# Kernel tuning notes

Hardware: AMD Instinct MI355X
Metric: run time of the kernel (lower is better)

The kernel has to match this reference:

```python
import jax, jax.numpy as jnp
import numpy as np

DIM = 768
HEADS = 12
HEAD_DIM = DIM // HEADS
EPS = 1e-5


def _layernorm(x, w, b):
    # normalize over last axis (head_dim), affine params shape [head_dim]
    mu = jnp.mean(x, axis=-1, keepdims=True)
    var = jnp.mean(jnp.square(x - mu), axis=-1, keepdims=True)
    return (x - mu) * jax.lax.rsqrt(var + EPS) * w + b


def setup_inputs() -> dict:
    key = jax.random.key(0)
    ks = jax.random.split(key, 8)
    B, N, C = 8, 1024, DIM
    s = 1.0 / np.sqrt(C)
    return {
        "x": jax.random.normal(ks[0], (B, N, C), jnp.float32),
        "qkv_w": jax.random.normal(ks[1], (3 * C, C), jnp.float32) * s,
        "qkv_b": jnp.zeros((3 * C,), jnp.float32),
        "qn_w": jnp.ones((HEAD_DIM,), jnp.float32),
        "qn_b": jnp.zeros((HEAD_DIM,), jnp.float32),
        "kn_w": jnp.ones((HEAD_DIM,), jnp.float32),
        "kn_b": jnp.zeros((HEAD_DIM,), jnp.float32),
        "proj_w": jax.random.normal(ks[2], (C, C), jnp.float32) * s,
        "proj_b": jnp.zeros((C,), jnp.float32),
    }


def reference(x, qkv_w, qkv_b, qn_w, qn_b, kn_w, kn_b, proj_w, proj_b):
    B, N, C = x.shape
    H, D = HEADS, HEAD_DIM
    scale = D ** -0.5
    # qkv projection: [B,N,3C] -> [3,B,H,N,D]
    qkv = (x @ qkv_w.T + qkv_b).reshape(B, N, 3, H, D).transpose(2, 0, 3, 1, 4)
    q, k, v = qkv[0], qkv[1], qkv[2]
    q = _layernorm(q, qn_w, qn_b)
    k = _layernorm(k, kn_w, kn_b)
    # attention scores [B,H,N,N]
    attn = jnp.einsum("bhqd,bhkd->bhqk", q, k) * scale
    attn = jax.nn.softmax(attn, axis=-1)
    out = jnp.einsum("bhqk,bhkd->bhqd", attn, v)  # [B,H,N,D]
    out = out.transpose(0, 2, 1, 3).reshape(B, N, C)
    return out @ proj_w.T + proj_b
```

## Files before the change

### kernel.cpp

```cpp
#include <hip/hip_runtime.h>

#define DIM 768
#define HEADS 12
#define HDIM 64
#define B_ 8
#define N_ 1024
#define EPS 1e-5f
#define QPRE 0.18033688f

typedef __bf16 bf16x8 __attribute__((ext_vector_type(8)));
typedef float  f32x4  __attribute__((ext_vector_type(4)));

using u16 = unsigned short;
using u32 = unsigned int;

static __device__ __forceinline__ u16 f2b_rne(float f){
    u32 u = __float_as_uint(f);
    u += 0x7fffu + ((u >> 16) & 1u);
    return (u16)(u >> 16);
}

static __device__ __forceinline__ void gl_lds16(const void* g, void* l){
    __builtin_amdgcn_global_load_lds(
        (const __attribute__((address_space(1))) unsigned int*)g,
        (__attribute__((address_space(3))) unsigned int*)l, 16, 0, 0);
}

__global__ __launch_bounds__(256) void cast_bf16_kernel(
    const float* __restrict__ in, u16* __restrict__ out, int n8)
{
    int i = blockIdx.x * 256 + threadIdx.x;
    if (i >= n8) return;
    const float4* p = (const float4*)in;
    float4 a = p[2*i], b = p[2*i+1];
    uint4 r;
    r.x = (u32)f2b_rne(a.x) | ((u32)f2b_rne(a.y) << 16);
    r.y = (u32)f2b_rne(a.z) | ((u32)f2b_rne(a.w) << 16);
    r.z = (u32)f2b_rne(b.x) | ((u32)f2b_rne(b.y) << 16);
    r.w = (u32)f2b_rne(b.z) | ((u32)f2b_rne(b.w) << 16);
    ((uint4*)out)[i] = r;
}

__global__ __launch_bounds__(256) void qkv_gemm_ln(
    const u16* __restrict__ xb, const u16* __restrict__ wb,
    const float* __restrict__ bias,
    const float* __restrict__ qn_w, const float* __restrict__ qn_b,
    const float* __restrict__ kn_w, const float* __restrict__ kn_b,
    u16* __restrict__ Q, u16* __restrict__ K, u16* __restrict__ VT)
{
    __shared__ __align__(16) unsigned char Asl[128*128];
    __shared__ __align__(16) unsigned char Bsl[128*128];
    const int t = threadIdx.x;
    const int lane = t & 63, wid = t >> 6;
    const int wr = wid >> 1, wc = wid & 1;
    const int l15 = lane & 15, l4 = lane >> 4;
    const int lr  = lane >> 3;
    const int lcs = ((lane & 7) ^ lr & 7) * 16;
    const int rsw = (l15 & 7) << 4;

    const int b0 = blockIdx.x;
    const int lg = (b0 & 7) * 144 + (b0 >> 3);
    const int col0 = (lg % 18) * 128, row0 = (lg / 18) * 128;

    f32x4 acc[4][4];
    #pragma unroll
    for (int m = 0; m < 4; ++m)
        #pragma unroll
        for (int n = 0; n < 4; ++n) acc[m][n] = f32x4{0.f,0.f,0.f,0.f};

    for (int k0 = 0; k0 < DIM; k0 += 64) {
        __syncthreads();
        #pragma unroll
        for (int c = 0; c < 4; ++c) {
            int rg = wid*32 + c*8;
            gl_lds16((const unsigned char*)xb + (size_t)(row0 + rg + lr)*1536 + k0*2 + lcs,
                     Asl + rg*128);
            gl_lds16((const unsigned char*)wb + (size_t)(col0 + rg + lr)*1536 + k0*2 + lcs,
                     Bsl + rg*128);
        }
        __syncthreads();
        #pragma unroll
        for (int s = 0; s < 2; ++s) {
            bf16x8 af[4], bfr[4];
            #pragma unroll
            for (int m = 0; m < 4; ++m)
                af[m] = *(const bf16x8*)(Asl + (wr*64 + m*16 + l15)*128 + ((l4*16 + s*64) ^ rsw));
            #pragma unroll
            for (int n = 0; n < 4; ++n)
                bfr[n] = *(const bf16x8*)(Bsl + (wc*64 + n*16 + l15)*128 + ((l4*16 + s*64) ^ rsw));
            #pragma unroll
            for (int m = 0; m < 4; ++m)
                #pragma unroll
                for (int n = 0; n < 4; ++n)
                    acc[m][n] = __builtin_amdgcn_mfma_f32_16x16x32_bf16(af[m], bfr[n], acc[m][n], 0, 0, 0);
        }
    }

    const int cg0 = col0 + wc*64;
    const int which = cg0 / DIM;
    const int h = (cg0 % DIM) / HDIM;

    float bias_v[4];
    #pragma unroll
    for (int n = 0; n < 4; ++n) bias_v[n] = bias[cg0 + n*16 + l15];
    #pragma unroll
    for (int m = 0; m < 4; ++m)
        #pragma unroll
        for (int n = 0; n < 4; ++n)
            #pragma unroll
            for (int r = 0; r < 4; ++r) acc[m][n][r] += bias_v[n];

    __syncthreads();
    unsigned char* Tw = (wid < 2 ? Asl : Bsl) + (wid & 1) * 8192;

    if (which < 2) {
        const float* lwp = (which == 0) ? qn_w : kn_w;
        const float* lbp = (which == 0) ? qn_b : kn_b;
        const float qsc = (which == 0) ? QPRE : 1.0f;
        float lw_v[4], lb_v[4];
        #pragma unroll
        for (int n = 0; n < 4; ++n) { lw_v[n] = lwp[n*16 + l15] * qsc; lb_v[n] = lbp[n*16 + l15] * qsc; }

        #pragma unroll
        for (int m = 0; m < 4; ++m)
            #pragma unroll
            for (int r = 0; r < 4; ++r) {
                float s = 0.f, s2 = 0.f;
                #pragma unroll
                for (int n = 0; n < 4; ++n) { float v = acc[m][n][r]; s += v; s2 += v*v; }
                #pragma unroll
                for (int off = 1; off < 16; off <<= 1) {
                    s  += __shfl_xor(s,  off, 64);
                    s2 += __shfl_xor(s2, off, 64);
                }
                float mu  = s * (1.f/64.f);
                float var = s2 * (1.f/64.f) - mu*mu;
                float rs  = rsqrtf(var + EPS);
                #pragma unroll
                for (int n = 0; n < 4; ++n)
                    acc[m][n][r] = (acc[m][n][r] - mu) * rs * lw_v[n] + lb_v[n];
            }

        #pragma unroll
        for (int m = 0; m < 4; ++m)
            #pragma unroll
            for (int n = 0; n < 4; ++n)
                #pragma unroll
                for (int r = 0; r < 4; ++r)
                    *(u16*)(Tw + (m*16 + l4*4 + r)*128 + (n*16 + l15)*2) = f2b_rne(acc[m][n][r]);

        u16* dst = (which == 0) ? Q : K;
        const int tok0 = row0 + wr*64;
        const int b = tok0 >> 10, n0 = tok0 & 1023;
        const size_t bh = (size_t)(b * HEADS + h);
        #pragma unroll
        for (int i = 0; i < 8; ++i) {
            int row = i*8 + (lane >> 3);
            int d0  = (lane & 7) * 8;
            uint4 val = *(const uint4*)(Tw + row*128 + d0*2);
            *(uint4*)(dst + (bh * N_ + n0 + row) * HDIM + d0) = val;
        }
    } else {
        #pragma unroll
        for (int n = 0; n < 4; ++n)
            #pragma unroll
            for (int m = 0; m < 4; ++m)
                #pragma unroll
                for (int r = 0; r < 4; ++r)
                    *(u16*)(Tw + (n*16 + l15)*128 + (m*16 + l4*4 + r)*2) = f2b_rne(acc[m][n][r]);

        const int tok0 = row0 + wr*64;
        const int b = tok0 >> 10, n0v = tok0 & 1023;
        const size_t bh = (size_t)(b * HEADS + h);
        #pragma unroll
        for (int i = 0; i < 8; ++i) {
            int d  = i*8 + (lane >> 3);
            int tk = (lane & 7) * 8;
            uint4 val = *(const uint4*)(Tw + d*128 + tk*2);
            *(uint4*)(VT + (bh * HDIM + d) * N_ + n0v + tk) = val;
        }
    }
}

__global__ __launch_bounds__(256) void attn_mfma(
    const u16* __restrict__ Q, const u16* __restrict__ K,
    const u16* __restrict__ VT, u16* __restrict__ A)
{
    __shared__ __align__(16) unsigned char Ks[2][64*128];
    __shared__ __align__(16) unsigned char Vs[2][64*128];
    __shared__ __align__(16) unsigned char Ps[4*16*144];
    const int t = threadIdx.x, lane = t & 63, w = t >> 6;
    const int l15 = lane & 15, l4 = lane >> 4;
    const int lr  = lane >> 3;
    const int lcs = ((lane & 7) ^ lr & 7) * 16;
    const int rsw = (l15 & 7) << 4;

    const int b0 = blockIdx.x;
    const int lg = (b0 & 7) * 192 + (b0 >> 3);
    const int qt = lg & 15, bh = lg >> 4;
    const size_t base = (size_t)bh * (N_ * HDIM);

    bf16x8 qa[2];
    {
        const unsigned char* qb = (const unsigned char*)(Q + base + (size_t)(qt*64 + w*16 + l15) * HDIM);
        qa[0] = *(const bf16x8*)(qb + l4*16);
        qa[1] = *(const bf16x8*)(qb + l4*16 + 64);
    }

    float l_run[4] = {0.f, 0.f, 0.f, 0.f};
    f32x4 o[4];
    #pragma unroll
    for (int n = 0; n < 4; ++n) o[n] = f32x4{0.f,0.f,0.f,0.f};

    unsigned char* Pw = Ps + w*2304;

    const unsigned char* kSrc = (const unsigned char*)K  + base*2 + (size_t)(w*16 + lr)*128  + lcs;
    const unsigned char* vSrc = (const unsigned char*)VT + base*2 + (size_t)(w*16 + lr)*2048 + lcs;
    unsigned char* kDst0 = Ks[0] + w*16*128;
    unsigned char* vDst0 = Vs[0] + w*16*128;

    auto stage = [&](int buf, int kt2){
        #pragma unroll
        for (int c = 0; c < 2; ++c) {
            gl_lds16(kSrc + (size_t)kt2*8192 + c*1024,  kDst0 + buf*8192 + c*1024);
            gl_lds16(vSrc + kt2*128 + c*16384,          vDst0 + buf*8192 + c*1024);
        }
    };

    stage(0, 0);
    __syncthreads();

    for (int kt = 0; kt < 16; ++kt) {
        const int cur = kt & 1;
        if (kt < 15) stage(cur ^ 1, kt + 1);

        f32x4 sv[4];
        #pragma unroll
        for (int n = 0; n < 4; ++n) {
            sv[n] = f32x4{0.f,0.f,0.f,0.f};
            #pragma unroll
            for (int s = 0; s < 2; ++s) {
                bf16x8 kb = *(const bf16x8*)(Ks[cur] + (n*16 + l15)*128 + ((l4*16 + s*64) ^ rsw));
                sv[n] = __builtin_amdgcn_mfma_f32_16x16x32_bf16(qa[s], kb, sv[n], 0, 0, 0);
            }
        }

        #pragma unroll
        for (int n = 0; n < 4; ++n)
            #pragma unroll
            for (int r = 0; r < 4; ++r) {
                float p = exp2f(sv[n][r]);
                l_run[r] += p;
                *(u16*)(Pw + (l4*4 + r)*144 + (n*16 + l15)*2) = f2b_rne(p);
            }

        bf16x8 pa0 = *(const bf16x8*)(Pw + l15*144 + l4*16);
        bf16x8 pa1 = *(const bf16x8*)(Pw + l15*144 + l4*16 + 64);
        #pragma unroll
        for (int n = 0; n < 4; ++n) {
            bf16x8 vb0 = *(const bf16x8*)(Vs[cur] + (n*16 + l15)*128 + ((l4*16) ^ rsw));
            o[n] = __builtin_amdgcn_mfma_f32_16x16x32_bf16(pa0, vb0, o[n], 0, 0, 0);
            bf16x8 vb1 = *(const bf16x8*)(Vs[cur] + (n*16 + l15)*128 + ((l4*16 + 64) ^ rsw));
            o[n] = __builtin_amdgcn_mfma_f32_16x16x32_bf16(pa1, vb1, o[n], 0, 0, 0);
        }

        __syncthreads();
    }

    #pragma unroll
    for (int off = 1; off < 16; off <<= 1)
        #pragma unroll
        for (int r = 0; r < 4; ++r) l_run[r] += __shfl_xor(l_run[r], off, 64);

    const int b = bh / HEADS, h = bh % HEADS;
    #pragma unroll
    for (int r = 0; r < 4; ++r) {
        float inv = 1.f / l_run[r];
        #pragma unroll
        for (int n = 0; n < 4; ++n)
            *(u16*)(Pw + (l4*4 + r)*132 + (n*16 + l15)*2) = f2b_rne(o[n][r] * inv);
    }
    #pragma unroll
    for (int i = 0; i < 2; ++i) {
        int row = i*8 + (lane >> 3);
        int d0  = (lane & 7) * 8;
        uint4 val = *(const uint4*)(Pw + row*132 + d0*2);
        int tok = qt*64 + w*16 + row;
        *(uint4*)(A + (((size_t)b * N_ + tok) * HEADS + h) * HDIM + d0) = val;
    }
}

__global__ __launch_bounds__(256) void proj_gemm(
    const u16* __restrict__ Ab, const u16* __restrict__ wb,
    const float* __restrict__ bias, float* __restrict__ out)
{
    __shared__ __align__(16) unsigned char Asl[128*128];
    __shared__ __align__(16) unsigned char Bsl[128*128];
    const int t = threadIdx.x;
    const int lane = t & 63, wid = t >> 6;
    const int wr = wid >> 1, wc = wid & 1;
    const int l15 = lane & 15, l4 = lane >> 4;
    const int lr  = lane >> 3;
    const int lcs = ((lane & 7) ^ lr & 7) * 16;
    const int rsw = (l15 & 7) << 4;

    const int b0 = blockIdx.x;
    const int lg = (b0 & 7) * 48 + (b0 >> 3);
    const int col0 = (lg % 6) * 128, row0 = (lg / 6) * 128;

    f32x4 acc[4][4];
    #pragma unroll
    for (int m = 0; m < 4; ++m)
        #pragma unroll
        for (int n = 0; n < 4; ++n) acc[m][n] = f32x4{0.f,0.f,0.f,0.f};

    for (int k0 = 0; k0 < DIM; k0 += 64) {
        __syncthreads();
        #pragma unroll
        for (int c = 0; c < 4; ++c) {
            int rg = wid*32 + c*8;
            gl_lds16((const unsigned char*)Ab + (size_t)(row0 + rg + lr)*1536 + k0*2 + lcs,
                     Asl + rg*128);
            gl_lds16((const unsigned char*)wb + (size_t)(col0 + rg + lr)*1536 + k0*2 + lcs,
                     Bsl + rg*128);
        }
        __syncthreads();
        #pragma unroll
        for (int s = 0; s < 2; ++s) {
            bf16x8 af[4], bfr[4];
            #pragma unroll
            for (int m = 0; m < 4; ++m)
                af[m] = *(const bf16x8*)(Asl + (wr*64 + m*16 + l15)*128 + ((l4*16 + s*64) ^ rsw));
            #pragma unroll
            for (int n = 0; n < 4; ++n)
                bfr[n] = *(const bf16x8*)(Bsl + (wc*64 + n*16 + l15)*128 + ((l4*16 + s*64) ^ rsw));
            #pragma unroll
            for (int m = 0; m < 4; ++m)
                #pragma unroll
                for (int n = 0; n < 4; ++n)
                    acc[m][n] = __builtin_amdgcn_mfma_f32_16x16x32_bf16(af[m], bfr[n], acc[m][n], 0, 0, 0);
        }
    }

    float bias_v[4];
    #pragma unroll
    for (int n = 0; n < 4; ++n) bias_v[n] = bias[col0 + wc*64 + n*16 + l15];
    #pragma unroll
    for (int m = 0; m < 4; ++m)
        #pragma unroll
        for (int r = 0; r < 4; ++r) {
            int rg = row0 + wr*64 + m*16 + l4*4 + r;
            #pragma unroll
            for (int n = 0; n < 4; ++n)
                out[(size_t)rg * DIM + col0 + wc*64 + n*16 + l15] = acc[m][n][r] + bias_v[n];
        }
}

extern "C" void kernel_launch(void* const* d_in, const int* in_sizes, int n_in,
                              void* d_out, int out_size, void* d_ws, size_t ws_size,
                              hipStream_t stream)
{
    const float* x      = (const float*)d_in[0];
    const float* qkv_w  = (const float*)d_in[1];
    const float* qkv_b  = (const float*)d_in[2];
    const float* qn_w   = (const float*)d_in[3];
    const float* qn_b   = (const float*)d_in[4];
    const float* kn_w   = (const float*)d_in[5];
    const float* kn_b   = (const float*)d_in[6];
    const float* proj_w = (const float*)d_in[7];
    const float* proj_b = (const float*)d_in[8];
    float* out = (float*)d_out;

    const size_t XE  = (size_t)B_ * N_ * DIM;
    const size_t QWE = (size_t)3 * DIM * DIM;
    const size_t PWE = (size_t)DIM * DIM;

    u16* xb  = (u16*)d_ws;
    u16* qwb = xb  + XE;
    u16* pwb = qwb + QWE;
    u16* Qb  = pwb + PWE;
    u16* Kb  = Qb  + XE;
    u16* VTb = Kb  + XE;
    u16* Ab  = VTb + XE;

    cast_bf16_kernel<<<(int)((XE/8  + 255)/256), 256, 0, stream>>>(x,      xb,  (int)(XE/8));
    cast_bf16_kernel<<<(int)((QWE/8 + 255)/256), 256, 0, stream>>>(qkv_w,  qwb, (int)(QWE/8));
    cast_bf16_kernel<<<(int)((PWE/8 + 255)/256), 256, 0, stream>>>(proj_w, pwb, (int)(PWE/8));

    qkv_gemm_ln<<<dim3(1152), 256, 0, stream>>>(xb, qwb, qkv_b, qn_w, qn_b,
                                                kn_w, kn_b, Qb, Kb, VTb);
    attn_mfma<<<dim3(1536), 256, 0, stream>>>(Qb, Kb, VTb, Ab);
    proj_gemm<<<dim3(384), 256, 0, stream>>>(Ab, pwb, proj_b, out);
}
```

Before: 151.0 us.

## Transpose attention MFMAs so each lane owns a query row, packing P writes

```diff
diff --git a/kernel.cpp b/kernel.cpp
--- a/kernel.cpp
+++ b/kernel.cpp
@@ -18,6 +18,12 @@
     u32 u = __float_as_uint(f);
     u += 0x7fffu + ((u >> 16) & 1u);
     return (u16)(u >> 16);
+}
+
+static __device__ __forceinline__ u32 cvt_pk_bf16(float lo, float hi){
+    u32 r;
+    asm("v_cvt_pk_bf16_f32 %0, %1, %2" : "=v"(r) : "v"(lo), "v"(hi));
+    return r;
 }
 
 static __device__ __forceinline__ void gl_lds16(const void* g, void* l){
@@ -188,12 +194,13 @@
 {
     __shared__ __align__(16) unsigned char Ks[2][64*128];
     __shared__ __align__(16) unsigned char Vs[2][64*128];
-    __shared__ __align__(16) unsigned char Ps[4*16*144];
+    __shared__ __align__(16) unsigned char Ps[4*2176];
     const int t = threadIdx.x, lane = t & 63, w = t >> 6;
     const int l15 = lane & 15, l4 = lane >> 4;
     const int lr  = lane >> 3;
     const int lcs = ((lane & 7) ^ lr & 7) * 16;
     const int rsw = (l15 & 7) << 4;
+    const int psw = (l15 & 7) << 4;
 
     const int b0 = blockIdx.x;
     const int lg = (b0 & 7) * 192 + (b0 >> 3);
@@ -207,12 +214,12 @@
         qa[1] = *(const bf16x8*)(qb + l4*16 + 64);
     }
 
-    float l_run[4] = {0.f, 0.f, 0.f, 0.f};
+    float l_run = 0.f;
     f32x4 o[4];
     #pragma unroll
-    for (int n = 0; n < 4; ++n) o[n] = f32x4{0.f,0.f,0.f,0.f};
-
-    unsigned char* Pw = Ps + w*2304;
+    for (int m = 0; m < 4; ++m) o[m] = f32x4{0.f,0.f,0.f,0.f};
+
+    unsigned char* Pw = Ps + w*2176;
 
     const unsigned char* kSrc = (const unsigned char*)K  + base*2 + (size_t)(w*16 + lr)*128  + lcs;
     const unsigned char* vSrc = (const unsigned char*)VT + base*2 + (size_t)(w*16 + lr)*2048 + lcs;
@@ -241,45 +248,44 @@
             #pragma unroll
             for (int s = 0; s < 2; ++s) {
                 bf16x8 kb = *(const bf16x8*)(Ks[cur] + (n*16 + l15)*128 + ((l4*16 + s*64) ^ rsw));
-                sv[n] = __builtin_amdgcn_mfma_f32_16x16x32_bf16(qa[s], kb, sv[n], 0, 0, 0);
+                sv[n] = __builtin_amdgcn_mfma_f32_16x16x32_bf16(kb, qa[s], sv[n], 0, 0, 0);
             }
         }
 
         #pragma unroll
-        for (int n = 0; n < 4; ++n)
-            #pragma unroll
-            for (int r = 0; r < 4; ++r) {
-                float p = exp2f(sv[n][r]);
-                l_run[r] += p;
-                *(u16*)(Pw + (l4*4 + r)*144 + (n*16 + l15)*2) = f2b_rne(p);
+        for (int n = 0; n < 4; ++n) {
+            float p0 = exp2f(sv[n][0]), p1 = exp2f(sv[n][1]);
+            float p2 = exp2f(sv[n][2]), p3 = exp2f(sv[n][3]);
+            l_run += (p0 + p1) + (p2 + p3);
+            uint2 pw;
+            pw.x = cvt_pk_bf16(p0, p1);
+            pw.y = cvt_pk_bf16(p2, p3);
+            *(uint2*)(Pw + l15*128 + ((n*32 + l4*8) ^ psw)) = pw;
+        }
+
+        #pragma unroll
+        for (int s = 0; s < 2; ++s) {
+            bf16x8 pb = *(const bf16x8*)(Pw + l15*128 + ((s*64 + l4*16) ^ psw));
+            #pragma unroll
+            for (int m = 0; m < 4; ++m) {
+                bf16x8 vb = *(const bf16x8*)(Vs[cur] + (m*16 + l15)*128 + ((l4*16 + s*64) ^ rsw));
+                o[m] = __builtin_amdgcn_mfma_f32_16x16x32_bf16(vb, pb, o[m], 0, 0, 0);
             }
-
-        bf16x8 pa0 = *(const bf16x8*)(Pw + l15*144 + l4*16);
-        bf16x8 pa1 = *(const bf16x8*)(Pw + l15*144 + l4*16 + 64);
-        #pragma unroll
-        for (int n = 0; n < 4; ++n) {
-            bf16x8 vb0 = *(const bf16x8*)(Vs[cur] + (n*16 + l15)*128 + ((l4*16) ^ rsw));
-            o[n] = __builtin_amdgcn_mfma_f32_16x16x32_bf16(pa0, vb0, o[n], 0, 0, 0);
-            bf16x8 vb1 = *(const bf16x8*)(Vs[cur] + (n*16 + l15)*128 + ((l4*16 + 64) ^ rsw));
-            o[n] = __builtin_amdgcn_mfma_f32_16x16x32_bf16(pa1, vb1, o[n], 0, 0, 0);
         }
 
         __syncthreads();
     }
 
-    #pragma unroll
-    for (int off = 1; off < 16; off <<= 1)
-        #pragma unroll
-        for (int r = 0; r < 4; ++r) l_run[r] += __shfl_xor(l_run[r], off, 64);
+    l_run += __shfl_xor(l_run, 16, 64);
+    l_run += __shfl_xor(l_run, 32, 64);
+    const float inv = 1.f / l_run;
 
     const int b = bh / HEADS, h = bh % HEADS;
     #pragma unroll
-    for (int r = 0; r < 4; ++r) {
-        float inv = 1.f / l_run[r];
-        #pragma unroll
-        for (int n = 0; n < 4; ++n)
-            *(u16*)(Pw + (l4*4 + r)*132 + (n*16 + l15)*2) = f2b_rne(o[n][r] * inv);
-    }
+    for (int m = 0; m < 4; ++m)
+        #pragma unroll
+        for (int r = 0; r < 4; ++r)
+            *(u16*)(Pw + l15*132 + (m*16 + l4*4 + r)*2) = f2b_rne(o[m][r] * inv);
     #pragma unroll
     for (int i = 0; i < 2; ++i) {
         int row = i*8 + (lane >> 3);
```

Result: faster. 144.9 us (-4.0%).
